# Kernel tuning notes

Measured on AMD Instinct MI355X. Metric: run time of the kernel, lower is better.

Reference implementation:

```python
import jax, jax.numpy as jnp
import numpy as np

BN_EPS = 1e-5

def _bn_train(x, g, b):
    # BatchNorm1d in training mode: biased batch stats over the row dim
    m = x.mean(0)
    v = x.var(0)
    return g * (x - m) * jax.lax.rsqrt(v + BN_EPS) + b


def setup_inputs() -> dict:
    key = jax.random.key(0)
    ks = jax.random.split(key, 16)
    N, V, C, H, T, NC, OD, EH, EC = 128, 128, 256, 512, 12, 5, 5, 256, 256
    s = 0.05
    idx = jax.random.randint(ks[1], (T, N), 0, NC)
    return {
        "x": jax.random.normal(ks[0], (N, V, C), jnp.float32),
        "hidden_states": jnp.zeros((N, V, H), jnp.float32),
        "cell_states": jnp.zeros((N, V, H), jnp.float32),
        "one_hots_c_pred_seq": jax.nn.one_hot(idx, NC, dtype=jnp.float32),
        "W_ih": jax.random.normal(ks[2], (4 * H, C), jnp.float32) * s,
        "W_hh": jax.random.normal(ks[3], (4 * H, H), jnp.float32) * s,
        "b_ih": jax.random.normal(ks[4], (4 * H,), jnp.float32) * s,
        "b_hh": jax.random.normal(ks[5], (4 * H,), jnp.float32) * s,
        "W_cls": jax.random.normal(ks[6], (NC, H), jnp.float32) * s,
        "b_cls": jax.random.normal(ks[7], (NC,), jnp.float32) * s,
        "W_eh": jax.random.normal(ks[8], (EH, H), jnp.float32) * s,
        "b_eh": jax.random.normal(ks[9], (EH,), jnp.float32) * s,
        "g_eh": jnp.ones((EH,), jnp.float32),
        "beta_eh": jnp.zeros((EH,), jnp.float32),
        "W_ec": jax.random.normal(ks[10], (EC, NC), jnp.float32) * s,
        "b_ec": jax.random.normal(ks[11], (EC,), jnp.float32) * s,
        "g_ec": jnp.ones((EC,), jnp.float32),
        "beta_ec": jnp.zeros((EC,), jnp.float32),
        "W_out": jax.random.normal(ks[12], (OD, EH + EC), jnp.float32) * s,
        "b_out": jax.random.normal(ks[13], (OD,), jnp.float32) * s,
    }


def reference(x, hidden_states, cell_states, one_hots_c_pred_seq,
              W_ih, W_hh, b_ih, b_hh, W_cls, b_cls,
              W_eh, b_eh, g_eh, beta_eh, W_ec, b_ec, g_ec, beta_ec,
              W_out, b_out):
    N, V, C = x.shape
    H = hidden_states.shape[-1]
    xf = x.reshape(N * V, C)
    gx = xf @ W_ih.T + b_ih  # input gates are identical every step (x is repeated)

    def step(carry, onehot):
        h, c = carry  # [N*V, H]
        gates = gx + h @ W_hh.T + b_hh
        i, f, g, o = jnp.split(gates, 4, axis=1)  # pytorch LSTMCell gate order
        c = jax.nn.sigmoid(f) * c + jax.nn.sigmoid(i) * jnp.tanh(g)
        h = jax.nn.sigmoid(o) * jnp.tanh(c)
        # ClassifierLayer: avg-pool over V then 1x1 conv == mean + linear
        oc = h.reshape(N, V, H).mean(1) @ W_cls.T + b_cls  # [N, nc]
        # PredictionLayer
        eh = jax.nn.relu(_bn_train(h @ W_eh.T + b_eh, g_eh, beta_eh))
        ohr = jnp.broadcast_to(onehot[:, None, :], (N, V, onehot.shape[-1])).reshape(N * V, -1)
        ec = jax.nn.relu(_bn_train(ohr @ W_ec.T + b_ec, g_ec, beta_ec))
        op = jnp.concatenate([eh, ec], axis=1) @ W_out.T + b_out  # [N*V, out_dim]
        return (h, c), (op.reshape(N, V, -1), oc)

    carry0 = (hidden_states.reshape(N * V, H), cell_states.reshape(N * V, H))
    _, (preds, c_outs) = jax.lax.scan(step, carry0, one_hots_c_pred_seq)
    preds = preds.transpose(1, 0, 2, 3)  # [N, T, V, out_dim]
    # output_activation: bivariate-Gaussian params
    pred_outs = jnp.stack([preds[..., 0], preds[..., 1],
                           jnp.exp(preds[..., 2]), jnp.exp(preds[..., 3]),
                           jnp.tanh(preds[..., 4])], axis=-1)
    return pred_outs, c_outs
```

## Files before the change

### kernel.cpp

```cpp
#include <hip/hip_runtime.h>
#include <hip/hip_bf16.h>
#include <stdint.h>

typedef __hip_bfloat16 bf16;
typedef __attribute__((ext_vector_type(8))) short bf16x8;
typedef __attribute__((ext_vector_type(4))) short bf16x4;
typedef __attribute__((ext_vector_type(4))) float f32x4;

#define NN 128
#define VV 128
#define CC 256
#define HH 512
#define TT 12
#define NCLS 5
#define OD 5
#define EHD 256
#define KCAT (HH + CC)
#define ROWS (NN * VV)
#define PRED_SZ (NN * TT * VV * OD)
#define LDP 72
#define MiB (1ull << 20)


__device__ __forceinline__ float sigm(float x) { return 1.f / (1.f + __expf(-x)); }
__device__ __forceinline__ float tanh_(float x) {
    x = fminf(fmaxf(x, -15.f), 15.f);
    float e = __expf(2.f * x);
    return (e - 1.f) / (e + 1.f);
}
__device__ __forceinline__ float bf2f(unsigned short v) {
    unsigned u = ((unsigned)v) << 16; float f; __builtin_memcpy(&f, &u, 4); return f;
}
__device__ __forceinline__ float ldin(const void* p, int i, int is32) {
    return is32 ? ((const float*)p)[i] : __bfloat162float(((const bf16*)p)[i]);
}

__global__ void detect_dtype(const void* g_eh, int* flag, int* hnz) {
    unsigned w = *(const unsigned*)g_eh;
    *flag = (w == 0x3F800000u) ? 1 : 0;
    *hnz = 0;
}

__global__ __launch_bounds__(256) void convert_in(const void* src, bf16* dst, int n, const int* flag) {
    int is32 = *flag;
    int i = blockIdx.x * 256 + threadIdx.x;
    int stride = gridDim.x * 256;
    if (is32) { const float* s = (const float*)src; for (; i < n; i += stride) dst[i] = __float2bfloat16(s[i]); }
    else      { const bf16*  s = (const bf16*)src;  for (; i < n; i += stride) dst[i] = s[i]; }
}

__global__ __launch_bounds__(256) void convert_in_hflag(const void* src, bf16* dst, int n, const int* flag,
                                                        int* nz) {
    int is32 = *flag;
    int i = blockIdx.x * 256 + threadIdx.x;
    int stride = gridDim.x * 256;
    int loc = 0;
    if (is32) {
        const float* s = (const float*)src;
        for (; i < n; i += stride) { float v = s[i]; if (__float_as_uint(v) != 0u) loc = 1; dst[i] = __float2bfloat16(v); }
    } else {
        const bf16* s = (const bf16*)src;
        for (; i < n; i += stride) { bf16 v = s[i]; if (*(const unsigned short*)&v) loc = 1; dst[i] = v; }
    }
    if (loc) atomicOr(nz, 1);
}

__global__ __launch_bounds__(256) void init_c(const void* cell, float* c, const int* flag) {
    int is32 = *flag;
    size_t i = (size_t)blockIdx.x * 256 + threadIdx.x;
    const size_t total = (size_t)ROWS * HH;
    for (; i < total; i += (size_t)8192 * 256) c[i] = ldin(cell, (int)i, is32);
}

__device__ __forceinline__ void issue_loads(const bf16* __restrict__ A, int lda, int row0, int ka,
                                            const bf16* __restrict__ B, int ldb, int col0, int kb,
                                            bf16x8 ar[4], bf16x8 br[4]) {
    int tid = threadIdx.x;
#pragma unroll
    for (int it = 0; it < 4; ++it) {
        int cidx = tid + 256 * it;
        int row = cidx >> 3;
        int cc8 = (cidx & 7) * 8;
        ar[it] = *(const bf16x8*)(A + (size_t)(row0 + row) * lda + ka + cc8);
        br[it] = *(const bf16x8*)(B + (size_t)(col0 + row) * ldb + kb + cc8);
    }
}
__device__ __forceinline__ void write_lds(bf16* As, bf16* Bs, const bf16x8 ar[4], const bf16x8 br[4]) {
    int tid = threadIdx.x;
#pragma unroll
    for (int it = 0; it < 4; ++it) {
        int cidx = tid + 256 * it;
        int row = cidx >> 3;
        int cc8 = (cidx & 7) * 8;
        *(bf16x8*)(As + row * LDP + cc8) = ar[it];
        *(bf16x8*)(Bs + row * LDP + cc8) = br[it];
    }
}

__device__ __forceinline__ void tile_mfma(const bf16* As, const bf16* Bs, f32x4 acc[4][4]) {
    const int lane = threadIdx.x & 63, wave = threadIdx.x >> 6;
    const int wro = (wave >> 1) * 64, wco = (wave & 1) * 64;
    const int l15 = lane & 15, l8 = (lane >> 4) * 8;
#pragma unroll
    for (int kk = 0; kk < 64; kk += 32) {
        bf16x8 af[4], bg[4];
#pragma unroll
        for (int x = 0; x < 4; ++x) {
            af[x] = *(const bf16x8*)(As + (wro + x * 16 + l15) * LDP + kk + l8);
            bg[x] = *(const bf16x8*)(Bs + (wco + x * 16 + l15) * LDP + kk + l8);
        }
#pragma unroll
        for (int bi = 0; bi < 4; ++bi)
#pragma unroll
            for (int bj = 0; bj < 4; ++bj)
                acc[bi][bj] = __builtin_amdgcn_mfma_f32_16x16x32_bf16(af[bi], bg[bj], acc[bi][bj], 0, 0, 0);
    }
}

__global__ __launch_bounds__(256) void prep_weights(const void* __restrict__ Wih, const void* __restrict__ Whh,
                                                    const void* __restrict__ bih, const void* __restrict__ bhh,
                                                    bf16* __restrict__ Wihp, bf16* __restrict__ Whhp,
                                                    float* __restrict__ biasp, const int* flag) {
    int is32 = *flag;
    int jg = blockIdx.x;
    int b = jg >> 7, j = jg & 127;
    int gate = (j >> 4) & 3;
    int unit = b * 32 + (j & 15) + 16 * (j >> 6);
    int p = gate * HH + unit;
    for (int k = threadIdx.x; k < HH; k += 256)
        Whhp[(size_t)jg * HH + k] = __float2bfloat16(ldin(Whh, p * HH + k, is32));
    for (int k = threadIdx.x; k < CC; k += 256)
        Wihp[(size_t)jg * CC + k] = __float2bfloat16(ldin(Wih, p * CC + k, is32));
    if (threadIdx.x == 0)
        biasp[jg] = ldin(bih, p, is32) + ldin(bhh, p, is32);
}

__global__ __launch_bounds__(256) void gemm_k0(const bf16* __restrict__ A, const bf16* __restrict__ B,
                                               const float* __restrict__ biasp, bf16* __restrict__ gx) {
    __shared__ bf16 As[128 * LDP], Bs[128 * LDP];
    f32x4 acc[4][4] = {};
    bf16x8 ar[4], br[4];
    int row0 = blockIdx.x * 128, col0 = blockIdx.y * 128;
    issue_loads(A, CC, row0, 0, B, CC, col0, 0, ar, br);
    for (int k0 = 0; k0 < CC; k0 += 64) {
        __syncthreads();
        write_lds(As, Bs, ar, br);
        __syncthreads();
        int kn = k0 + 64;
        if (kn < CC) issue_loads(A, CC, row0, kn, B, CC, col0, kn, ar, br);
        tile_mfma(As, Bs, acc);
    }
    int lane = threadIdx.x & 63, wave = threadIdx.x >> 6;
    int wro = (wave >> 1) * 64, wco = (wave & 1) * 64;
    int l15 = lane & 15, lr4 = (lane >> 4) * 4;
#pragma unroll
    for (int bj = 0; bj < 4; ++bj) {
        int j = wco + bj * 16 + l15;
        float bia = biasp[col0 + j];
        int sidx = wco + l15 * 4 + bj;
#pragma unroll
        for (int bi = 0; bi < 4; ++bi)
#pragma unroll
            for (int reg = 0; reg < 4; ++reg) {
                int r = row0 + wro + bi * 16 + lr4 + reg;
                gx[(size_t)r * 2048 + col0 + sidx] = __float2bfloat16(acc[bi][bj][reg] + bia);
            }
    }
}

__global__ __launch_bounds__(256) void ec_precompute(const void* __restrict__ W_ec, const void* __restrict__ b_ec,
                                                     const void* __restrict__ g_ec, const void* __restrict__ beta_ec,
                                                     const void* __restrict__ W_out, const void* __restrict__ b_out,
                                                     const void* __restrict__ onehot, float* __restrict__ ecd_all,
                                                     const int* flag) {
    __shared__ float ecv[NCLS][EHD];
    __shared__ float cntf[NCLS];
    __shared__ float ecdc[NCLS][OD];
    int is32 = *flag;
    int t = blockIdx.x, tid = threadIdx.x;
    int ohoff = t * NN * NCLS;
    if (tid < NCLS) {
        float cnum = 0.f;
        for (int n = 0; n < NN; ++n) cnum += ldin(onehot, ohoff + n * NCLS + tid, is32);
        cntf[tid] = cnum * (1.f / NN);
    }
    __syncthreads();
    {
        int j = tid;
        float vals[NCLS];
        float m = 0.f, e2 = 0.f;
        float be = ldin(b_ec, j, is32);
        for (int cc = 0; cc < NCLS; ++cc) {
            vals[cc] = ldin(W_ec, j * NCLS + cc, is32) + be;
            m += cntf[cc] * vals[cc];
            e2 += cntf[cc] * vals[cc] * vals[cc];
        }
        float rs = rsqrtf(e2 - m * m + 1e-5f);
        float g = ldin(g_ec, j, is32), bt = ldin(beta_ec, j, is32);
        for (int cc = 0; cc < NCLS; ++cc)
            ecv[cc][j] = fmaxf(g * (vals[cc] - m) * rs + bt, 0.f);
    }
    __syncthreads();
    if (tid < NCLS * OD) {
        int cc = tid / OD, k = tid % OD;
        float s = 0.f;
        for (int j = 0; j < EHD; ++j) s += ecv[cc][j] * ldin(W_out, k * (EHD * 2) + EHD + j, is32);
        ecdc[cc][k] = s;
    }
    __syncthreads();
    if (tid < NN) {
        for (int k = 0; k < OD; ++k) {
            float s = ldin(b_out, k, is32);
            for (int cc = 0; cc < NCLS; ++cc) s += ldin(onehot, ohoff + tid * NCLS + cc, is32) * ecdc[cc][k];
            ecd_all[((size_t)t * NN + tid) * OD + k] = s;
        }
    }
}

__global__ __launch_bounds__(256) void lstm_gemm_gx(const bf16* __restrict__ h_in, const bf16* __restrict__ Whhp,
                                                    const bf16* __restrict__ gx, float* __restrict__ c,
                                                    bf16* __restrict__ h_out, float* __restrict__ csum,
                                                    float* __restrict__ colsum, float* __restrict__ colss) {
    __shared__ bf16 As[128 * LDP], Bs[128 * LDP];
    __shared__ float hsum[32];
    f32x4 acc[4][4] = {};
    bf16x8 ar[4], br[4];
    bf16x4 gpre[16];
    float  cpre[16];
    int row0 = blockIdx.x * 128, col0 = blockIdx.y * 128;
    int tid = threadIdx.x, lane = tid & 63, wave = tid >> 6;
    int wro = (wave >> 1) * 64;
    int l15 = lane & 15, lr4 = (lane >> 4) * 4;
    int ul = (wave & 1) * 16 + l15;
    int u = blockIdx.y * 32 + ul;
    const bf16* gxp = gx + col0 + (wave & 1) * 64 + l15 * 4;
    issue_loads(h_in, HH, row0, 0, Whhp, HH, col0, 0, ar, br);
#pragma unroll
    for (int k0 = 0; k0 < HH; k0 += 64) {
        __syncthreads();
        write_lds(As, Bs, ar, br);
        __syncthreads();
        int kn = k0 + 64;
        if (kn < HH) issue_loads(h_in, HH, row0, kn, Whhp, HH, col0, kn, ar, br);
#pragma unroll
        for (int e = 0; e < 2; ++e) {
            int idx = (k0 >> 6) * 2 + e;
            int bi = idx >> 2, reg = idx & 3;
            int r = row0 + wro + bi * 16 + lr4 + reg;
            gpre[idx] = *(const bf16x4*)(gxp + (size_t)r * 2048);
            cpre[idx] = c[(size_t)r * HH + u];
        }
        tile_mfma(As, Bs, acc);
    }
    if (tid < 32) hsum[tid] = 0.f;
    if (blockIdx.x == 0 && blockIdx.y == 0) { colsum[tid & 255] = 0.f; colss[tid & 255] = 0.f; }
    __syncthreads();
    float hpart = 0.f;
#pragma unroll
    for (int bi = 0; bi < 4; ++bi) {
#pragma unroll
        for (int reg = 0; reg < 4; ++reg) {
            int idx = bi * 4 + reg;
            int r = row0 + wro + bi * 16 + lr4 + reg;
            float gi = acc[bi][0][reg] + bf2f((unsigned short)gpre[idx][0]);
            float gf = acc[bi][1][reg] + bf2f((unsigned short)gpre[idx][1]);
            float gg = acc[bi][2][reg] + bf2f((unsigned short)gpre[idx][2]);
            float go = acc[bi][3][reg] + bf2f((unsigned short)gpre[idx][3]);
            float iv = sigm(gi), fv = sigm(gf), gv = tanh_(gg), ov = sigm(go);
            size_t ci = (size_t)r * HH + u;
            float cn = fv * cpre[idx] + iv * gv;
            c[ci] = cn;
            float hv = ov * tanh_(cn);
            h_out[ci] = __float2bfloat16(hv);
            hpart += hv;
        }
    }
    atomicAdd(&hsum[ul], hpart);
    __syncthreads();
    if (tid < 32) csum[(size_t)blockIdx.x * HH + blockIdx.y * 32 + tid] = hsum[tid];
}

__global__ __launch_bounds__(256) void lstm_gemm_gx_first(const bf16* __restrict__ h_in, const bf16* __restrict__ Whhp,
                                                          const bf16* __restrict__ gx, float* __restrict__ c,
                                                          bf16* __restrict__ h_out, float* __restrict__ csum,
                                                          float* __restrict__ colsum, float* __restrict__ colss,
                                                          const int* __restrict__ gemm_flag) {
    __shared__ bf16 As[128 * LDP], Bs[128 * LDP];
    __shared__ float hsum[32];
    f32x4 acc[4][4] = {};
    bf16x8 ar[4], br[4];
    bf16x4 gpre[16];
    float  cpre[16];
    int row0 = blockIdx.x * 128, col0 = blockIdx.y * 128;
    int tid = threadIdx.x, lane = tid & 63, wave = tid >> 6;
    int wro = (wave >> 1) * 64;
    int l15 = lane & 15, lr4 = (lane >> 4) * 4;
    int ul = (wave & 1) * 16 + l15;
    int u = blockIdx.y * 32 + ul;
    const bf16* gxp = gx + col0 + (wave & 1) * 64 + l15 * 4;
    const int do_gemm = *gemm_flag;
    if (do_gemm) {
        issue_loads(h_in, HH, row0, 0, Whhp, HH, col0, 0, ar, br);
#pragma unroll
        for (int k0 = 0; k0 < HH; k0 += 64) {
            __syncthreads();
            write_lds(As, Bs, ar, br);
            __syncthreads();
            int kn = k0 + 64;
            if (kn < HH) issue_loads(h_in, HH, row0, kn, Whhp, HH, col0, kn, ar, br);
#pragma unroll
            for (int e = 0; e < 2; ++e) {
                int idx = (k0 >> 6) * 2 + e;
                int bi = idx >> 2, reg = idx & 3;
                int r = row0 + wro + bi * 16 + lr4 + reg;
                gpre[idx] = *(const bf16x4*)(gxp + (size_t)r * 2048);
                cpre[idx] = c[(size_t)r * HH + u];
            }
            tile_mfma(As, Bs, acc);
        }
    } else {
#pragma unroll
        for (int idx = 0; idx < 16; ++idx) {
            int bi = idx >> 2, reg = idx & 3;
            int r = row0 + wro + bi * 16 + lr4 + reg;
            gpre[idx] = *(const bf16x4*)(gxp + (size_t)r * 2048);
            cpre[idx] = c[(size_t)r * HH + u];
        }
    }
    if (tid < 32) hsum[tid] = 0.f;
    if (blockIdx.x == 0 && blockIdx.y == 0) { colsum[tid & 255] = 0.f; colss[tid & 255] = 0.f; }
    __syncthreads();
    float hpart = 0.f;
#pragma unroll
    for (int bi = 0; bi < 4; ++bi) {
#pragma unroll
        for (int reg = 0; reg < 4; ++reg) {
            int idx = bi * 4 + reg;
            int r = row0 + wro + bi * 16 + lr4 + reg;
            float gi = acc[bi][0][reg] + bf2f((unsigned short)gpre[idx][0]);
            float gf = acc[bi][1][reg] + bf2f((unsigned short)gpre[idx][1]);
            float gg = acc[bi][2][reg] + bf2f((unsigned short)gpre[idx][2]);
            float go = acc[bi][3][reg] + bf2f((unsigned short)gpre[idx][3]);
            float iv = sigm(gi), fv = sigm(gf), gv = tanh_(gg), ov = sigm(go);
            size_t ci = (size_t)r * HH + u;
            float cn = fv * cpre[idx] + iv * gv;
            c[ci] = cn;
            float hv = ov * tanh_(cn);
            h_out[ci] = __float2bfloat16(hv);
            hpart += hv;
        }
    }
    atomicAdd(&hsum[ul], hpart);
    __syncthreads();
    if (tid < 32) csum[(size_t)blockIdx.x * HH + blockIdx.y * 32 + tid] = hsum[tid];
}

__global__ __launch_bounds__(256) void lstm_gemm_cat(const bf16* __restrict__ h_in, const bf16* __restrict__ x,
                                                     const bf16* __restrict__ Wihp, const bf16* __restrict__ Whhp,
                                                     const float* __restrict__ biasp, float* __restrict__ c,
                                                     bf16* __restrict__ h_out, float* __restrict__ csum,
                                                     float* __restrict__ colsum, float* __restrict__ colss) {
    __shared__ bf16 As[128 * LDP], Bs[128 * LDP];
    __shared__ float hsum[32];
    f32x4 acc[4][4] = {};
    bf16x8 ar[4], br[4];
    int row0 = blockIdx.x * 128, col0 = blockIdx.y * 128;
    issue_loads(h_in, HH, row0, 0, Whhp, HH, col0, 0, ar, br);
    for (int k0 = 0; k0 < KCAT; k0 += 64) {
        __syncthreads();
        write_lds(As, Bs, ar, br);
        __syncthreads();
        int kn = k0 + 64;
        if (kn < KCAT) {
            if (kn < HH) issue_loads(h_in, HH, row0, kn, Whhp, HH, col0, kn, ar, br);
            else         issue_loads(x, CC, row0, kn - HH, Wihp, CC, col0, kn - HH, ar, br);
        }
        tile_mfma(As, Bs, acc);
    }
    int tid = threadIdx.x;
    if (tid < 32) hsum[tid] = 0.f;
    if (blockIdx.x == 0 && blockIdx.y == 0) { colsum[tid & 255] = 0.f; colss[tid & 255] = 0.f; }
    __syncthreads();
    int lane = tid & 63, wave = tid >> 6;
    int wro = (wave >> 1) * 64;
    int l15 = lane & 15, lr4 = (lane >> 4) * 4;
    int ul = (wave & 1) * 16 + l15;
    int u = blockIdx.y * 32 + ul;
    int colp = col0 + (wave & 1) * 64 + l15;
    float b0 = biasp[colp], b1 = biasp[colp + 16], b2 = biasp[colp + 32], b3 = biasp[colp + 48];
    float hpart = 0.f;
#pragma unroll
    for (int bi = 0; bi < 4; ++bi) {
#pragma unroll
        for (int reg = 0; reg < 4; ++reg) {
            int r = row0 + wro + bi * 16 + lr4 + reg;
            float gi = acc[bi][0][reg] + b0;
            float gf = acc[bi][1][reg] + b1;
            float gg = acc[bi][2][reg] + b2;
            float go = acc[bi][3][reg] + b3;
            float iv = sigm(gi), fv = sigm(gf), gv = tanh_(gg), ov = sigm(go);
            size_t ci = (size_t)r * HH + u;
            float cn = fv * c[ci] + iv * gv;
            c[ci] = cn;
            float hv = ov * tanh_(cn);
            h_out[ci] = __float2bfloat16(hv);
            hpart += hv;
        }
    }
    atomicAdd(&hsum[ul], hpart);
    __syncthreads();
    if (tid < 32) csum[(size_t)blockIdx.x * HH + blockIdx.y * 32 + tid] = hsum[tid];
}

__global__ __launch_bounds__(256) void eh_cls(const bf16* __restrict__ A, const bf16* __restrict__ B,
                                              const void* __restrict__ bias, bf16* __restrict__ out,
                                              float* __restrict__ colsum, float* __restrict__ colss,
                                              const float* __restrict__ csum, const void* __restrict__ W_cls,
                                              const void* __restrict__ b_cls, void* __restrict__ outp,
                                              int t, const int* flag) {
    int is32 = *flag;
    int tid = threadIdx.x;
    if (blockIdx.x >= 512) {
        __shared__ float wl[NCLS * HH];
        __shared__ float wred[4][NCLS];
        int wave = tid >> 6, lane = tid & 63;
        for (int i = tid; i < NCLS * HH; i += 256) wl[i] = ldin(W_cls, i, is32);
        __syncthreads();
        int n = blockIdx.x - 512;
        float pk[NCLS] = {};
        for (int u = tid; u < HH; u += 256) {
            float cv = csum[(size_t)n * HH + u];
#pragma unroll
            for (int k = 0; k < NCLS; ++k) pk[k] += cv * wl[k * HH + u];
        }
#pragma unroll
        for (int off = 32; off; off >>= 1)
#pragma unroll
            for (int k = 0; k < NCLS; ++k) pk[k] += __shfl_down(pk[k], off, 64);
        if (lane == 0)
#pragma unroll
            for (int k = 0; k < NCLS; ++k) wred[wave][k] = pk[k];
        __syncthreads();
        if (tid < NCLS) {
            float a = (wred[0][tid] + wred[1][tid] + wred[2][tid] + wred[3][tid]) * (1.f / VV) + ldin(b_cls, tid, is32);
            int idx = PRED_SZ + t * (NN * NCLS) + n * NCLS + tid;
            if (is32) ((float*)outp)[idx] = a;
            else      ((bf16*)outp)[idx] = __float2bfloat16(a);
        }
        return;
    }
    __shared__ bf16 As[64 * LDP], Bs[128 * LDP];
    __shared__ float s_sum[128], s_ss[128];
    f32x4 acc[4][2] = {};
    bf16x8 ar[2], br[4];
    int row0 = (blockIdx.x >> 1) * 64, col0 = (blockIdx.x & 1) * 128;
#pragma unroll
    for (int it = 0; it < 2; ++it) { int cx = tid + 256 * it; ar[it] = *(const bf16x8*)(A + (size_t)(row0 + (cx >> 3)) * HH + (cx & 7) * 8); }
#pragma unroll
    for (int it = 0; it < 4; ++it) { int cx = tid + 256 * it; br[it] = *(const bf16x8*)(B + (size_t)(col0 + (cx >> 3)) * HH + (cx & 7) * 8); }
    const int lane = tid & 63, wave = tid >> 6;
    const int l15 = lane & 15, l8 = (lane >> 4) * 8;
    for (int k0 = 0; k0 < HH; k0 += 64) {
        __syncthreads();
#pragma unroll
        for (int it = 0; it < 2; ++it) { int cx = tid + 256 * it; *(bf16x8*)(As + (cx >> 3) * LDP + (cx & 7) * 8) = ar[it]; }
#pragma unroll
        for (int it = 0; it < 4; ++it) { int cx = tid + 256 * it; *(bf16x8*)(Bs + (cx >> 3) * LDP + (cx & 7) * 8) = br[it]; }
        __syncthreads();
        int kn = k0 + 64;
        if (kn < HH) {
#pragma unroll
            for (int it = 0; it < 2; ++it) { int cx = tid + 256 * it; ar[it] = *(const bf16x8*)(A + (size_t)(row0 + (cx >> 3)) * HH + kn + (cx & 7) * 8); }
#pragma unroll
            for (int it = 0; it < 4; ++it) { int cx = tid + 256 * it; br[it] = *(const bf16x8*)(B + (size_t)(col0 + (cx >> 3)) * HH + kn + (cx & 7) * 8); }
        }
#pragma unroll
        for (int kk = 0; kk < 64; kk += 32) {
            bf16x8 af[4], bg[2];
#pragma unroll
            for (int x = 0; x < 4; ++x) af[x] = *(const bf16x8*)(As + (x * 16 + l15) * LDP + kk + l8);
#pragma unroll
            for (int x = 0; x < 2; ++x) bg[x] = *(const bf16x8*)(Bs + (wave * 32 + x * 16 + l15) * LDP + kk + l8);
#pragma unroll
            for (int bi = 0; bi < 4; ++bi)
#pragma unroll
                for (int bj = 0; bj < 2; ++bj)
                    acc[bi][bj] = __builtin_amdgcn_mfma_f32_16x16x32_bf16(af[bi], bg[bj], acc[bi][bj], 0, 0, 0);
        }
    }
    int lr4 = (lane >> 4) * 4;
    if (tid < 128) { s_sum[tid] = 0.f; s_ss[tid] = 0.f; }
    __syncthreads();
#pragma unroll
    for (int bj = 0; bj < 2; ++bj) {
        int j = wave * 32 + bj * 16 + l15;
        int col = col0 + j;
        float bia = ldin(bias, col, is32);
        float ps = 0.f, pss = 0.f;
#pragma unroll
        for (int bi = 0; bi < 4; ++bi)
#pragma unroll
            for (int reg = 0; reg < 4; ++reg) {
                int r = row0 + bi * 16 + lr4 + reg;
                float val = acc[bi][bj][reg] + bia;
                out[(size_t)r * EHD + col] = __float2bfloat16(val);
                ps += val; pss += val * val;
            }
        atomicAdd(&s_sum[j], ps);
        atomicAdd(&s_ss[j], pss);
    }
    __syncthreads();
    if (tid < 128) {
        atomicAdd(&colsum[col0 + tid], s_sum[tid]);
        atomicAdd(&colss[col0 + tid], s_ss[tid]);
    }
}

__global__ __launch_bounds__(256) void final_kernel(const bf16* __restrict__ eh_pre, const float* __restrict__ colsum,
                                                    const float* __restrict__ colss, const void* __restrict__ g_eh,
                                                    const void* __restrict__ beta_eh, const void* __restrict__ W_out,
                                                    const float* __restrict__ ecd_all, void* __restrict__ out,
                                                    int t, const int* flag) {
    __shared__ float Wl[OD * EHD];
    int is32 = *flag;
    for (int i = threadIdx.x; i < OD * EHD; i += 256)
        Wl[i] = ldin(W_out, (i >> 8) * (EHD * 2) + (i & 255), is32);
    __syncthreads();
    int wave = threadIdx.x >> 6, lane = threadIdx.x & 63;
    int r = blockIdx.x * 4 + wave;
    int j0 = lane * 4;
    const float4 cs = *(const float4*)(colsum + j0);
    const float4 sq = *(const float4*)(colss + j0);
    float av[4], bv[4];
    const float* csp = (const float*)&cs;
    const float* sqp = (const float*)&sq;
#pragma unroll
    for (int e = 0; e < 4; ++e) {
        float mean = csp[e] * (1.f / ROWS);
        float var = sqp[e] * (1.f / ROWS) - mean * mean;
        float a = ldin(g_eh, j0 + e, is32) * rsqrtf(var + 1e-5f);
        av[e] = a;
        bv[e] = ldin(beta_eh, j0 + e, is32) - mean * a;
    }
    bf16x4 xs = *(const bf16x4*)(eh_pre + (size_t)r * EHD + j0);
    float v0 = fmaxf(av[0] * bf2f((unsigned short)xs[0]) + bv[0], 0.f);
    float v1 = fmaxf(av[1] * bf2f((unsigned short)xs[1]) + bv[1], 0.f);
    float v2 = fmaxf(av[2] * bf2f((unsigned short)xs[2]) + bv[2], 0.f);
    float v3 = fmaxf(av[3] * bf2f((unsigned short)xs[3]) + bv[3], 0.f);
    float p[OD];
#pragma unroll
    for (int k = 0; k < OD; ++k)
        p[k] = v0 * Wl[k * EHD + j0] + v1 * Wl[k * EHD + j0 + 1] + v2 * Wl[k * EHD + j0 + 2] + v3 * Wl[k * EHD + j0 + 3];
#pragma unroll
    for (int off = 32; off; off >>= 1)
#pragma unroll
        for (int k = 0; k < OD; ++k) p[k] += __shfl_down(p[k], off, 64);
    if (lane == 0) {
        int n = r >> 7, v = r & 127;
        const float* en = ecd_all + ((size_t)t * NN + n) * OD;
        float o0 = p[0] + en[0];
        float o1 = p[1] + en[1];
        float o2 = expf(p[2] + en[2]);
        float o3 = expf(p[3] + en[3]);
        float o4 = tanh_(p[4] + en[4]);
        size_t base = (size_t)n * (TT * VV * OD) + (size_t)t * (VV * OD) + (size_t)v * OD;
        if (is32) {
            float* dst = (float*)out + base;
            dst[0] = o0; dst[1] = o1; dst[2] = o2; dst[3] = o3; dst[4] = o4;
        } else {
            bf16* dst = (bf16*)out + base;
            dst[0] = __float2bfloat16(o0);
            dst[1] = __float2bfloat16(o1);
            dst[2] = __float2bfloat16(o2);
            dst[3] = __float2bfloat16(o3);
            dst[4] = __float2bfloat16(o4);
        }
    }
}

extern "C" void kernel_launch(void* const* d_in, const int* in_sizes, int n_in,
                              void* d_out, int out_size, void* d_ws, size_t ws_size,
                              hipStream_t stream) {
    const void* x       = d_in[0];
    const void* hidden  = d_in[1];
    const void* cell    = d_in[2];
    const void* onehot  = d_in[3];
    const void* W_ih    = d_in[4];
    const void* W_hh    = d_in[5];
    const void* b_ih    = d_in[6];
    const void* b_hh    = d_in[7];
    const void* W_cls   = d_in[8];
    const void* b_cls   = d_in[9];
    const void* W_eh    = d_in[10];
    const void* b_eh    = d_in[11];
    const void* g_eh    = d_in[12];
    const void* beta_eh = d_in[13];
    const void* W_ec    = d_in[14];
    const void* b_ec    = d_in[15];
    const void* g_ec    = d_in[16];
    const void* beta_ec = d_in[17];
    const void* W_out   = d_in[18];
    const void* b_out   = d_in[19];

    const int use_gx = (ws_size >= 148 * MiB) ? 1 : 0;

    char* ws = (char*)d_ws;
    float* cbuf = (float*)(ws);
    bf16*  h0   = (bf16*)(ws + 32 * MiB);
    bf16*  h1   = (bf16*)(ws + 48 * MiB);
    bf16*  gxb  = (bf16*)(ws + 64 * MiB);
    bf16*  ehp, *x_c, *Wihp, *Whhp, *Weh_c;
    char*  tail;
    if (use_gx) {
        ehp   = (bf16*)(ws + 128 * MiB);
        x_c   = (bf16*)(ws + 136 * MiB);
        Wihp  = (bf16*)(ws + 144 * MiB);
        Whhp  = (bf16*)(ws + 145 * MiB);
        Weh_c = (bf16*)(ws + 147 * MiB);
        tail  = ws + 147 * MiB + 524288;
    } else {
        ehp   = (bf16*)(ws + 64 * MiB);
        x_c   = (bf16*)(ws + 72 * MiB);
        Wihp  = (bf16*)(ws + 80 * MiB);
        Whhp  = (bf16*)(ws + 81 * MiB);
        Weh_c = (bf16*)(ws + 83 * MiB);
        tail  = ws + 83 * MiB + 524288;
    }
    float* biasp   = (float*)(tail);
    float* colsum  = (float*)(tail + 8192);
    float* colss   = (float*)(tail + 9216);
    int*   dflag   = (int*)  (tail + 16384);
    int*   hnz     = (int*)  (tail + 16388);
    float* csum    = (float*)(tail + 20480);
    float* ecd_all = (float*)(tail + 20480 + 262144);

    detect_dtype<<<1, 1, 0, stream>>>(g_eh, dflag, hnz);
    convert_in<<<4096, 256, 0, stream>>>(x, x_c, ROWS * CC, dflag);
    convert_in_hflag<<<4096, 256, 0, stream>>>(hidden, h0, ROWS * HH, dflag, hnz);
    convert_in<<<512, 256, 0, stream>>>(W_eh, Weh_c, EHD * HH, dflag);
    init_c<<<8192, 256, 0, stream>>>(cell, cbuf, dflag);
    prep_weights<<<2048, 256, 0, stream>>>(W_ih, W_hh, b_ih, b_hh, Wihp, Whhp, biasp, dflag);
    ec_precompute<<<TT, 256, 0, stream>>>(W_ec, b_ec, g_ec, beta_ec, W_out, b_out, onehot, ecd_all, dflag);
    if (use_gx)
        gemm_k0<<<dim3(128, 16), 256, 0, stream>>>(x_c, Wihp, biasp, gxb);

    for (int t = 0; t < TT; ++t) {
        const bf16* hin = (t & 1) ? h1 : h0;
        bf16* hout = (t & 1) ? h0 : h1;
        if (use_gx) {
            if (t == 0)
                lstm_gemm_gx_first<<<dim3(128, 16), 256, 0, stream>>>(hin, Whhp, gxb, cbuf, hout, csum, colsum, colss, hnz);
            else
                lstm_gemm_gx<<<dim3(128, 16), 256, 0, stream>>>(hin, Whhp, gxb, cbuf, hout, csum, colsum, colss);
        } else {
            lstm_gemm_cat<<<dim3(128, 16), 256, 0, stream>>>(hin, x_c, Wihp, Whhp, biasp, cbuf, hout, csum, colsum, colss);
        }
        eh_cls<<<640, 256, 0, stream>>>(hout, Weh_c, b_eh, ehp, colsum, colss,
                                        csum, W_cls, b_cls, d_out, t, dflag);
        final_kernel<<<4096, 256, 0, stream>>>(ehp, colsum, colss, g_eh, beta_eh, W_out, ecd_all, d_out, t, dflag);
    }
}
```

Baseline: 1.320 ms.

## Fold previous step's BN/output pass into next step's eh_cls launch

The per-step final_kernel (BatchNorm apply, ReLU, output projection) for step t-1 now runs as 1024 extra blocks appended to step t's eh_cls grid. The pre-activation buffer and the column sum and sum-of-squares buffers are double-buffered so both steps can be in flight at once. Only the last step still gets a standalone final_kernel launch. This removes eleven kernel launches and lets the memory-bound epilogue overlap with the next step's GEMM blocks. The cost is a larger workspace, reuse of the x_c region as a second buffer, and a heavier eh_cls kernel whose shared-memory use now covers three roles.

After: 1.278 ms. -3.2%, faster.

```diff
diff --git a/kernel.cpp b/kernel.cpp
--- a/kernel.cpp
+++ b/kernel.cpp
@@ -412,137 +412,23 @@
     if (tid < 32) csum[(size_t)blockIdx.x * HH + blockIdx.y * 32 + tid] = hsum[tid];
 }
 
-__global__ __launch_bounds__(256) void eh_cls(const bf16* __restrict__ A, const bf16* __restrict__ B,
-                                              const void* __restrict__ bias, bf16* __restrict__ out,
-                                              float* __restrict__ colsum, float* __restrict__ colss,
-                                              const float* __restrict__ csum, const void* __restrict__ W_cls,
-                                              const void* __restrict__ b_cls, void* __restrict__ outp,
-                                              int t, const int* flag) {
-    int is32 = *flag;
-    int tid = threadIdx.x;
-    if (blockIdx.x >= 512) {
-        __shared__ float wl[NCLS * HH];
-        __shared__ float wred[4][NCLS];
-        int wave = tid >> 6, lane = tid & 63;
-        for (int i = tid; i < NCLS * HH; i += 256) wl[i] = ldin(W_cls, i, is32);
-        __syncthreads();
-        int n = blockIdx.x - 512;
-        float pk[NCLS] = {};
-        for (int u = tid; u < HH; u += 256) {
-            float cv = csum[(size_t)n * HH + u];
-#pragma unroll
-            for (int k = 0; k < NCLS; ++k) pk[k] += cv * wl[k * HH + u];
-        }
-#pragma unroll
-        for (int off = 32; off; off >>= 1)
-#pragma unroll
-            for (int k = 0; k < NCLS; ++k) pk[k] += __shfl_down(pk[k], off, 64);
-        if (lane == 0)
-#pragma unroll
-            for (int k = 0; k < NCLS; ++k) wred[wave][k] = pk[k];
-        __syncthreads();
-        if (tid < NCLS) {
-            float a = (wred[0][tid] + wred[1][tid] + wred[2][tid] + wred[3][tid]) * (1.f / VV) + ldin(b_cls, tid, is32);
-            int idx = PRED_SZ + t * (NN * NCLS) + n * NCLS + tid;
-            if (is32) ((float*)outp)[idx] = a;
-            else      ((bf16*)outp)[idx] = __float2bfloat16(a);
-        }
-        return;
-    }
-    __shared__ bf16 As[64 * LDP], Bs[128 * LDP];
-    __shared__ float s_sum[128], s_ss[128];
-    f32x4 acc[4][2] = {};
-    bf16x8 ar[2], br[4];
-    int row0 = (blockIdx.x >> 1) * 64, col0 = (blockIdx.x & 1) * 128;
-#pragma unroll
-    for (int it = 0; it < 2; ++it) { int cx = tid + 256 * it; ar[it] = *(const bf16x8*)(A + (size_t)(row0 + (cx >> 3)) * HH + (cx & 7) * 8); }
-#pragma unroll
-    for (int it = 0; it < 4; ++it) { int cx = tid + 256 * it; br[it] = *(const bf16x8*)(B + (size_t)(col0 + (cx >> 3)) * HH + (cx & 7) * 8); }
-    const int lane = tid & 63, wave = tid >> 6;
-    const int l15 = lane & 15, l8 = (lane >> 4) * 8;
-    for (int k0 = 0; k0 < HH; k0 += 64) {
-        __syncthreads();
-#pragma unroll
-        for (int it = 0; it < 2; ++it) { int cx = tid + 256 * it; *(bf16x8*)(As + (cx >> 3) * LDP + (cx & 7) * 8) = ar[it]; }
-#pragma unroll
-        for (int it = 0; it < 4; ++it) { int cx = tid + 256 * it; *(bf16x8*)(Bs + (cx >> 3) * LDP + (cx & 7) * 8) = br[it]; }
-        __syncthreads();
-        int kn = k0 + 64;
-        if (kn < HH) {
-#pragma unroll
-            for (int it = 0; it < 2; ++it) { int cx = tid + 256 * it; ar[it] = *(const bf16x8*)(A + (size_t)(row0 + (cx >> 3)) * HH + kn + (cx & 7) * 8); }
-#pragma unroll
-            for (int it = 0; it < 4; ++it) { int cx = tid + 256 * it; br[it] = *(const bf16x8*)(B + (size_t)(col0 + (cx >> 3)) * HH + kn + (cx & 7) * 8); }
-        }
-#pragma unroll
-        for (int kk = 0; kk < 64; kk += 32) {
-            bf16x8 af[4], bg[2];
-#pragma unroll
-            for (int x = 0; x < 4; ++x) af[x] = *(const bf16x8*)(As + (x * 16 + l15) * LDP + kk + l8);
-#pragma unroll
-            for (int x = 0; x < 2; ++x) bg[x] = *(const bf16x8*)(Bs + (wave * 32 + x * 16 + l15) * LDP + kk + l8);
-#pragma unroll
-            for (int bi = 0; bi < 4; ++bi)
-#pragma unroll
-                for (int bj = 0; bj < 2; ++bj)
-                    acc[bi][bj] = __builtin_amdgcn_mfma_f32_16x16x32_bf16(af[bi], bg[bj], acc[bi][bj], 0, 0, 0);
-        }
-    }
-    int lr4 = (lane >> 4) * 4;
-    if (tid < 128) { s_sum[tid] = 0.f; s_ss[tid] = 0.f; }
-    __syncthreads();
-#pragma unroll
-    for (int bj = 0; bj < 2; ++bj) {
-        int j = wave * 32 + bj * 16 + l15;
-        int col = col0 + j;
-        float bia = ldin(bias, col, is32);
-        float ps = 0.f, pss = 0.f;
-#pragma unroll
-        for (int bi = 0; bi < 4; ++bi)
-#pragma unroll
-            for (int reg = 0; reg < 4; ++reg) {
-                int r = row0 + bi * 16 + lr4 + reg;
-                float val = acc[bi][bj][reg] + bia;
-                out[(size_t)r * EHD + col] = __float2bfloat16(val);
-                ps += val; pss += val * val;
-            }
-        atomicAdd(&s_sum[j], ps);
-        atomicAdd(&s_ss[j], pss);
-    }
-    __syncthreads();
-    if (tid < 128) {
-        atomicAdd(&colsum[col0 + tid], s_sum[tid]);
-        atomicAdd(&colss[col0 + tid], s_ss[tid]);
-    }
-}
-
-__global__ __launch_bounds__(256) void final_kernel(const bf16* __restrict__ eh_pre, const float* __restrict__ colsum,
-                                                    const float* __restrict__ colss, const void* __restrict__ g_eh,
-                                                    const void* __restrict__ beta_eh, const void* __restrict__ W_out,
-                                                    const float* __restrict__ ecd_all, void* __restrict__ out,
-                                                    int t, const int* flag) {
-    __shared__ float Wl[OD * EHD];
-    int is32 = *flag;
-    for (int i = threadIdx.x; i < OD * EHD; i += 256)
-        Wl[i] = ldin(W_out, (i >> 8) * (EHD * 2) + (i & 255), is32);
-    __syncthreads();
+__device__ __forceinline__ void final_rows(int grp, const bf16* __restrict__ ehp, const float* __restrict__ colsum,
+                                           const float* __restrict__ colss, const void* __restrict__ g_eh,
+                                           const void* __restrict__ beta_eh, const float* __restrict__ ecd_all,
+                                           const float* Wl, void* __restrict__ out, int t, int is32) {
     int wave = threadIdx.x >> 6, lane = threadIdx.x & 63;
-    int r = blockIdx.x * 4 + wave;
+    int r = grp * 4 + wave;
     int j0 = lane * 4;
-    const float4 cs = *(const float4*)(colsum + j0);
-    const float4 sq = *(const float4*)(colss + j0);
     float av[4], bv[4];
-    const float* csp = (const float*)&cs;
-    const float* sqp = (const float*)&sq;
 #pragma unroll
     for (int e = 0; e < 4; ++e) {
-        float mean = csp[e] * (1.f / ROWS);
-        float var = sqp[e] * (1.f / ROWS) - mean * mean;
+        float mean = colsum[j0 + e] * (1.f / ROWS);
+        float var = colss[j0 + e] * (1.f / ROWS) - mean * mean;
         float a = ldin(g_eh, j0 + e, is32) * rsqrtf(var + 1e-5f);
         av[e] = a;
         bv[e] = ldin(beta_eh, j0 + e, is32) - mean * a;
     }
-    bf16x4 xs = *(const bf16x4*)(eh_pre + (size_t)r * EHD + j0);
+    bf16x4 xs = *(const bf16x4*)(ehp + (size_t)r * EHD + j0);
     float v0 = fmaxf(av[0] * bf2f((unsigned short)xs[0]) + bv[0], 0.f);
     float v1 = fmaxf(av[1] * bf2f((unsigned short)xs[1]) + bv[1], 0.f);
     float v2 = fmaxf(av[2] * bf2f((unsigned short)xs[2]) + bv[2], 0.f);
@@ -576,6 +462,140 @@
             dst[4] = __float2bfloat16(o4);
         }
     }
+}
+
+__global__ __launch_bounds__(256) void eh_cls(const bf16* __restrict__ A, const bf16* __restrict__ B,
+                                              const void* __restrict__ bias, bf16* __restrict__ out,
+                                              float* __restrict__ colsum, float* __restrict__ colss,
+                                              const float* __restrict__ csum, const void* __restrict__ W_cls,
+                                              const void* __restrict__ b_cls, void* __restrict__ outp,
+                                              int t, const int* flag,
+                                              const bf16* __restrict__ ehp_prev, const float* __restrict__ colsum_prev,
+                                              const float* __restrict__ colss_prev, const void* __restrict__ g_eh,
+                                              const void* __restrict__ beta_eh, const void* __restrict__ W_out,
+                                              const float* __restrict__ ecd_all, int tprev) {
+    int is32 = *flag;
+    int tid = threadIdx.x;
+    if (blockIdx.x >= 640) {
+        if (tprev < 0) return;
+        __shared__ float Wl[OD * EHD];
+        for (int i = tid; i < OD * EHD; i += 256)
+            Wl[i] = ldin(W_out, (i >> 8) * (EHD * 2) + (i & 255), is32);
+        __syncthreads();
+        int b = blockIdx.x - 640;
+#pragma unroll
+        for (int g = 0; g < 4; ++g)
+            final_rows(b * 4 + g, ehp_prev, colsum_prev, colss_prev, g_eh, beta_eh,
+                       ecd_all, Wl, outp, tprev, is32);
+        return;
+    }
+    if (blockIdx.x >= 512) {
+        __shared__ float wl[NCLS * HH];
+        __shared__ float wred[4][NCLS];
+        int wave = tid >> 6, lane = tid & 63;
+        for (int i = tid; i < NCLS * HH; i += 256) wl[i] = ldin(W_cls, i, is32);
+        __syncthreads();
+        int n = blockIdx.x - 512;
+        float pk[NCLS] = {};
+        for (int u = tid; u < HH; u += 256) {
+            float cv = csum[(size_t)n * HH + u];
+#pragma unroll
+            for (int k = 0; k < NCLS; ++k) pk[k] += cv * wl[k * HH + u];
+        }
+#pragma unroll
+        for (int off = 32; off; off >>= 1)
+#pragma unroll
+            for (int k = 0; k < NCLS; ++k) pk[k] += __shfl_down(pk[k], off, 64);
+        if (lane == 0)
+#pragma unroll
+            for (int k = 0; k < NCLS; ++k) wred[wave][k] = pk[k];
+        __syncthreads();
+        if (tid < NCLS) {
+            float a = (wred[0][tid] + wred[1][tid] + wred[2][tid] + wred[3][tid]) * (1.f / VV) + ldin(b_cls, tid, is32);
+            int idx = PRED_SZ + t * (NN * NCLS) + n * NCLS + tid;
+            if (is32) ((float*)outp)[idx] = a;
+            else      ((bf16*)outp)[idx] = __float2bfloat16(a);
+        }
+        return;
+    }
+    __shared__ bf16 As[64 * LDP], Bs[128 * LDP];
+    __shared__ float s_sum[128], s_ss[128];
+    f32x4 acc[4][2] = {};
+    bf16x8 ar[2], br[4];
+    int row0 = (blockIdx.x >> 1) * 64, col0 = (blockIdx.x & 1) * 128;
+#pragma unroll
+    for (int it = 0; it < 2; ++it) { int cx = tid + 256 * it; ar[it] = *(const bf16x8*)(A + (size_t)(row0 + (cx >> 3)) * HH + (cx & 7) * 8); }
+#pragma unroll
+    for (int it = 0; it < 4; ++it) { int cx = tid + 256 * it; br[it] = *(const bf16x8*)(B + (size_t)(col0 + (cx >> 3)) * HH + (cx & 7) * 8); }
+    const int lane = tid & 63, wave = tid >> 6;
+    const int l15 = lane & 15, l8 = (lane >> 4) * 8;
+    for (int k0 = 0; k0 < HH; k0 += 64) {
+        __syncthreads();
+#pragma unroll
+        for (int it = 0; it < 2; ++it) { int cx = tid + 256 * it; *(bf16x8*)(As + (cx >> 3) * LDP + (cx & 7) * 8) = ar[it]; }
+#pragma unroll
+        for (int it = 0; it < 4; ++it) { int cx = tid + 256 * it; *(bf16x8*)(Bs + (cx >> 3) * LDP + (cx & 7) * 8) = br[it]; }
+        __syncthreads();
+        int kn = k0 + 64;
+        if (kn < HH) {
+#pragma unroll
+            for (int it = 0; it < 2; ++it) { int cx = tid + 256 * it; ar[it] = *(const bf16x8*)(A + (size_t)(row0 + (cx >> 3)) * HH + kn + (cx & 7) * 8); }
+#pragma unroll
+            for (int it = 0; it < 4; ++it) { int cx = tid + 256 * it; br[it] = *(const bf16x8*)(B + (size_t)(col0 + (cx >> 3)) * HH + kn + (cx & 7) * 8); }
+        }
+#pragma unroll
+        for (int kk = 0; kk < 64; kk += 32) {
+            bf16x8 af[4], bg[2];
+#pragma unroll
+            for (int x = 0; x < 4; ++x) af[x] = *(const bf16x8*)(As + (x * 16 + l15) * LDP + kk + l8);
+#pragma unroll
+            for (int x = 0; x < 2; ++x) bg[x] = *(const bf16x8*)(Bs + (wave * 32 + x * 16 + l15) * LDP + kk + l8);
+#pragma unroll
+            for (int bi = 0; bi < 4; ++bi)
+#pragma unroll
+                for (int bj = 0; bj < 2; ++bj)
+                    acc[bi][bj] = __builtin_amdgcn_mfma_f32_16x16x32_bf16(af[bi], bg[bj], acc[bi][bj], 0, 0, 0);
+        }
+    }
+    int lr4 = (lane >> 4) * 4;
+    if (tid < 128) { s_sum[tid] = 0.f; s_ss[tid] = 0.f; }
+    __syncthreads();
+#pragma unroll
+    for (int bj = 0; bj < 2; ++bj) {
+        int j = wave * 32 + bj * 16 + l15;
+        int col = col0 + j;
+        float bia = ldin(bias, col, is32);
+        float ps = 0.f, pss = 0.f;
+#pragma unroll
+        for (int bi = 0; bi < 4; ++bi)
+#pragma unroll
+            for (int reg = 0; reg < 4; ++reg) {
+                int r = row0 + bi * 16 + lr4 + reg;
+                float val = acc[bi][bj][reg] + bia;
+                out[(size_t)r * EHD + col] = __float2bfloat16(val);
+                ps += val; pss += val * val;
+            }
+        atomicAdd(&s_sum[j], ps);
+        atomicAdd(&s_ss[j], pss);
+    }
+    __syncthreads();
+    if (tid < 128) {
+        atomicAdd(&colsum[col0 + tid], s_sum[tid]);
+        atomicAdd(&colss[col0 + tid], s_ss[tid]);
+    }
+}
+
+__global__ __launch_bounds__(256) void final_kernel(const bf16* __restrict__ eh_pre, const float* __restrict__ colsum,
+                                                    const float* __restrict__ colss, const void* __restrict__ g_eh,
+                                                    const void* __restrict__ beta_eh, const void* __restrict__ W_out,
+                                                    const float* __restrict__ ecd_all, void* __restrict__ out,
+                                                    int t, const int* flag) {
+    __shared__ float Wl[OD * EHD];
+    int is32 = *flag;
+    for (int i = threadIdx.x; i < OD * EHD; i += 256)
+        Wl[i] = ldin(W_out, (i >> 8) * (EHD * 2) + (i & 255), is32);
+    __syncthreads();
+    final_rows(blockIdx.x, eh_pre, colsum, colss, g_eh, beta_eh, ecd_all, Wl, out, t, is32);
 }
 
 extern "C" void kernel_launch(void* const* d_in, const int* in_sizes, int n_in,
@@ -609,30 +629,38 @@
     bf16*  h0   = (bf16*)(ws + 32 * MiB);
     bf16*  h1   = (bf16*)(ws + 48 * MiB);
     bf16*  gxb  = (bf16*)(ws + 64 * MiB);
-    bf16*  ehp, *x_c, *Wihp, *Whhp, *Weh_c;
+    bf16*  ehp0, *ehp1, *x_c, *Wihp, *Whhp, *Weh_c;
     char*  tail;
     if (use_gx) {
-        ehp   = (bf16*)(ws + 128 * MiB);
+        ehp0  = (bf16*)(ws + 128 * MiB);
         x_c   = (bf16*)(ws + 136 * MiB);
+        ehp1  = (bf16*)(ws + 136 * MiB);
         Wihp  = (bf16*)(ws + 144 * MiB);
         Whhp  = (bf16*)(ws + 145 * MiB);
         Weh_c = (bf16*)(ws + 147 * MiB);
         tail  = ws + 147 * MiB + 524288;
     } else {
-        ehp   = (bf16*)(ws + 64 * MiB);
+        ehp0  = (bf16*)(ws + 64 * MiB);
         x_c   = (bf16*)(ws + 72 * MiB);
-        Wihp  = (bf16*)(ws + 80 * MiB);
-        Whhp  = (bf16*)(ws + 81 * MiB);
-        Weh_c = (bf16*)(ws + 83 * MiB);
-        tail  = ws + 83 * MiB + 524288;
+        ehp1  = (bf16*)(ws + 80 * MiB);
+        Wihp  = (bf16*)(ws + 88 * MiB);
+        Whhp  = (bf16*)(ws + 89 * MiB);
+        Weh_c = (bf16*)(ws + 91 * MiB);
+        tail  = ws + 91 * MiB + 524288;
     }
     float* biasp   = (float*)(tail);
-    float* colsum  = (float*)(tail + 8192);
-    float* colss   = (float*)(tail + 9216);
+    float* colsum0 = (float*)(tail + 8192);
+    float* colss0  = (float*)(tail + 9216);
+    float* colsum1 = (float*)(tail + 10240);
+    float* colss1  = (float*)(tail + 11264);
     int*   dflag   = (int*)  (tail + 16384);
     int*   hnz     = (int*)  (tail + 16388);
     float* csum    = (float*)(tail + 20480);
     float* ecd_all = (float*)(tail + 20480 + 262144);
+
+    bf16*  ehp_b[2]    = { ehp0, ehp1 };
+    float* colsum_b[2] = { colsum0, colsum1 };
+    float* colss_b[2]  = { colss0, colss1 };
 
     detect_dtype<<<1, 1, 0, stream>>>(g_eh, dflag, hnz);
     convert_in<<<4096, 256, 0, stream>>>(x, x_c, ROWS * CC, dflag);
@@ -647,16 +675,23 @@
     for (int t = 0; t < TT; ++t) {
         const bf16* hin = (t & 1) ? h1 : h0;
         bf16* hout = (t & 1) ? h0 : h1;
+        int cur = t & 1, prv = (t - 1) & 1;
         if (use_gx) {
             if (t == 0)
-                lstm_gemm_gx_first<<<dim3(128, 16), 256, 0, stream>>>(hin, Whhp, gxb, cbuf, hout, csum, colsum, colss, hnz);
+                lstm_gemm_gx_first<<<dim3(128, 16), 256, 0, stream>>>(hin, Whhp, gxb, cbuf, hout, csum,
+                                                                      colsum_b[cur], colss_b[cur], hnz);
             else
-                lstm_gemm_gx<<<dim3(128, 16), 256, 0, stream>>>(hin, Whhp, gxb, cbuf, hout, csum, colsum, colss);
+                lstm_gemm_gx<<<dim3(128, 16), 256, 0, stream>>>(hin, Whhp, gxb, cbuf, hout, csum,
+                                                                colsum_b[cur], colss_b[cur]);
         } else {
-            lstm_gemm_cat<<<dim3(128, 16), 256, 0, stream>>>(hin, x_c, Wihp, Whhp, biasp, cbuf, hout, csum, colsum, colss);
-        }
-        eh_cls<<<640, 256, 0, stream>>>(hout, Weh_c, b_eh, ehp, colsum, colss,
-                                        csum, W_cls, b_cls, d_out, t, dflag);
-        final_kernel<<<4096, 256, 0, stream>>>(ehp, colsum, colss, g_eh, beta_eh, W_out, ecd_all, d_out, t, dflag);
-    }
-}
+            lstm_gemm_cat<<<dim3(128, 16), 256, 0, stream>>>(hin, x_c, Wihp, Whhp, biasp, cbuf, hout, csum,
+                                                             colsum_b[cur], colss_b[cur]);
+        }
+        eh_cls<<<1664, 256, 0, stream>>>(hout, Weh_c, b_eh, ehp_b[cur], colsum_b[cur], colss_b[cur],
+                                         csum, W_cls, b_cls, d_out, t, dflag,
+                                         ehp_b[prv], colsum_b[prv], colss_b[prv], g_eh, beta_eh,
+                                         W_out, ecd_all, t - 1);
+    }
+    final_kernel<<<4096, 256, 0, stream>>>(ehp_b[(TT - 1) & 1], colsum_b[(TT - 1) & 1], colss_b[(TT - 1) & 1],
+                                           g_eh, beta_eh, W_out, ecd_all, d_out, TT - 1, dflag);
+}
```
